# Performance work log

Measured on AMD Instinct MI355X. Metric: run time of the kernel, lower is better.

## Reference

```python
import jax, jax.numpy as jnp
import numpy as np

B, D_IN, H, D_OUT = 2048, 1024, 2048, 1024
MAX_STEPS = 12
EPS = 0.01


def setup_inputs() -> dict:
    key = jax.random.key(0)
    ks = jax.random.split(key, 8)
    s_in = 1.0 / np.sqrt(D_IN + H)
    s_h = 1.0 / np.sqrt(H)
    return {
        "x": jax.random.normal(ks[0], (B, D_IN), jnp.float32),
        "h": jax.random.normal(ks[1], (B, H), jnp.float32),
        "W_hidden": jax.random.normal(ks[2], (H, D_IN + H), jnp.float32) * s_in,
        "b_hidden": jnp.zeros((H,), jnp.float32),
        "w_halt": jax.random.normal(ks[3], (H,), jnp.float32) * s_h,
        "b_halt": jnp.float32(-2.0),  # bias low so several ponder steps are taken
        "W_out": jax.random.normal(ks[4], (D_OUT, H), jnp.float32) * s_h,
        "b_out": jnp.zeros((D_OUT,), jnp.float32),
    }


def reference(x, h, W_hidden, b_hidden, w_halt, b_halt, W_out, b_out):
    # Batched ACT halting loop, unrolled to MAX_STEPS via lax.scan.
    def step(s, t):
        # step 0 of the original uses x+1 as a "first step" flag
        xin = jnp.where(t == 0, x + 1.0, x)          # [B, D_IN]
        z = jnp.concatenate([xin, s], axis=-1)        # [B, D_IN+H]
        s_new = z @ W_hidden.T + b_hidden             # [B, H]
        p = jax.nn.sigmoid(s_new @ w_halt + b_halt)   # [B]
        out = s_new @ W_out.T + b_out                 # [B, D_OUT]
        return s_new, (s_new, p, out)

    _, (states, probs, outs) = jax.lax.scan(step, h, jnp.arange(MAX_STEPS))
    # states: [T,B,H], probs: [T,B], outs: [T,B,D_OUT]

    cum = jnp.cumsum(probs, axis=0)                   # [T,B]
    reached = cum >= (1.0 - EPS)
    # first step where cumulative halt prob crosses the threshold (cap at T-1)
    n = jnp.where(jnp.any(reached, axis=0), jnp.argmax(reached, axis=0), MAX_STEPS - 1)  # [B]

    t_idx = jnp.arange(MAX_STEPS)[:, None]            # [T,1]
    before = t_idx < n[None, :]                       # [T,B]
    R = 1.0 - jnp.sum(jnp.where(before, probs, 0.0), axis=0)  # [B] remainder
    w = jnp.where(before, probs, jnp.where(t_idx == n[None, :], R[None, :], 0.0))  # [T,B]

    output = jnp.einsum("tb,tbd->bd", w, outs)        # [B, D_OUT]
    hidden = jnp.einsum("tb,tbh->bh", w, states)      # [B, H]
    ponder = (n + 1).astype(jnp.float32) + R          # [B]
    return output, hidden, ponder
```

## Files before the change

kernel.cpp:

```cpp
#include <hip/hip_runtime.h>
#include <hip/hip_bf16.h>
#include <cstdint>

#define B_SZ   2048
#define D_INN  1024
#define H_SZ   2048
#define D_OUTN 1024
#define TMAX   12
#define LDW    3072

typedef _Float16 f16;
typedef __attribute__((ext_vector_type(8))) _Float16 f16x8;
typedef __attribute__((ext_vector_type(4))) float    f32x4;

typedef const __attribute__((address_space(1))) uint32_t* gptr_t;
typedef __attribute__((address_space(3))) uint32_t*       lptr_t;
__device__ inline void gld16(const void* g, void* l) {
    __builtin_amdgcn_global_load_lds((gptr_t)g, (lptr_t)l, 16, 0, 0);
}

template<int BN>
__global__ __launch_bounds__(512, 4) void gemm16(
    const f16* __restrict__ A, int lda,
    const f16* __restrict__ Bm, int ldb,
    const float* __restrict__ Cadd,
    const float* __restrict__ radd,
    float* __restrict__ Cf,
    f16* __restrict__ Cs,
    float* __restrict__ hid,
    const float* __restrict__ wvec,
    int hacc,
    f16* __restrict__ hid16,
    int ldc, int K, int nx)
{
    constexpr int WN = BN / 64;
    constexpr int NV = (BN == 128) ? 3 : 2;
    __shared__ __align__(16) f16 As[3][64 * 64];
    __shared__ __align__(16) f16 Bs[3][BN * 64];
    const int tid  = threadIdx.x;
    const int wave = tid >> 6;
    const int lane = tid & 63;

    const int nwg = gridDim.x;
    const int cpx = nwg >> 3;
    const int bid = (blockIdx.x & 7) * cpx + (blockIdx.x >> 3);
    const int m0 = (bid / nx) * 64, n0 = (bid % nx) * BN;

    const int wr = wave >> 2, wc = wave & 3;
    const int fr = lane & 15, fq = lane >> 4;

    const int acs = tid ^ ((tid >> 3) & 7);
    const f16* gA = A + (size_t)(m0 + (acs >> 3)) * lda + (acs & 7) * 8;
    const int adst = wave << 9;
    const int bcs1 = tid ^ ((tid >> 3) & 7);
    const f16* gB1 = Bm + (size_t)(n0 + (bcs1 >> 3)) * ldb + (bcs1 & 7) * 8;
    const int bdst1 = wave << 9;
    const f16* gB2 = nullptr;
    int bdst2 = 0;
    if constexpr (BN == 128) {
        const int bc2 = tid + 512;
        const int bcs2 = bc2 ^ ((bc2 >> 3) & 7);
        gB2 = Bm + (size_t)(n0 + (bcs2 >> 3)) * ldb + (bcs2 & 7) * 8;
        bdst2 = 4096 + (wave << 9);
    }

    int offA[2][2], offB[WN][2];
#pragma unroll
    for (int m = 0; m < 2; ++m)
#pragma unroll
        for (int ks = 0; ks < 2; ++ks) {
            const int row = wr * 32 + m * 16 + fr;
            offA[m][ks] = row * 64 + (((ks * 4 + fq) ^ (row & 7)) << 3);
        }
#pragma unroll
    for (int n = 0; n < WN; ++n)
#pragma unroll
        for (int ks = 0; ks < 2; ++ks) {
            const int row = wc * (WN * 16) + n * 16 + fr;
            offB[n][ks] = row * 64 + (((ks * 4 + fq) ^ (row & 7)) << 3);
        }

    auto STAGE = [&](int buf, int ko) {
        gld16(gA + ko,  &As[buf][0] + adst);
        gld16(gB1 + ko, &Bs[buf][0] + bdst1);
        if constexpr (BN == 128) gld16(gB2 + ko, &Bs[buf][0] + bdst2);
    };

    f32x4 acc[2][WN] = {};

    STAGE(0, 0);
    const int nk = K >> 6;
    int cur = 0;
    for (int ki = 0; ki < nk; ++ki) {
        const int nxt = (cur == 2) ? 0 : cur + 1;
        if (ki + 1 < nk) {
            STAGE(nxt, (ki + 1) << 6);
            asm volatile("s_waitcnt vmcnt(%0)" :: "i"(NV) : "memory");
        } else {
            asm volatile("s_waitcnt vmcnt(0)" ::: "memory");
        }
        __builtin_amdgcn_s_barrier();
        asm volatile("" ::: "memory");

        f16x8 a[2][2], b[WN][2];
#pragma unroll
        for (int m = 0; m < 2; ++m)
#pragma unroll
            for (int ks = 0; ks < 2; ++ks)
                a[m][ks] = *(const f16x8*)(&As[cur][offA[m][ks]]);
#pragma unroll
        for (int n = 0; n < WN; ++n)
#pragma unroll
            for (int ks = 0; ks < 2; ++ks)
                b[n][ks] = *(const f16x8*)(&Bs[cur][offB[n][ks]]);
#pragma unroll
        for (int ks = 0; ks < 2; ++ks)
#pragma unroll
            for (int m = 0; m < 2; ++m)
#pragma unroll
                for (int n = 0; n < WN; ++n)
                    acc[m][n] = __builtin_amdgcn_mfma_f32_16x16x32_f16(
                        a[m][ks], b[n][ks], acc[m][n], 0, 0, 0);
        cur = nxt;
    }

    float wr8[2][4];
    if (hid) {
#pragma unroll
        for (int m = 0; m < 2; ++m)
#pragma unroll
            for (int r = 0; r < 4; ++r)
                wr8[m][r] = wvec[m0 + wr * 32 + m * 16 + fq * 4 + r];
    }
#pragma unroll
    for (int m = 0; m < 2; ++m) {
#pragma unroll
        for (int n = 0; n < WN; ++n) {
#pragma unroll
            for (int r = 0; r < 4; ++r) {
                const int row = m0 + wr * 32 + m * 16 + fq * 4 + r;
                const int col = n0 + wc * (WN * 16) + n * 16 + fr;
                const size_t o = (size_t)row * ldc + col;
                float v = acc[m][n][r];
                if (Cadd) v += Cadd[o];
                if (radd) v += radd[col];
                if (Cf) Cf[o] = v;
                if (Cs) Cs[o] = (f16)v;
                if (hid) {
                    const float hv = hacc ? hid[o] + wr8[m][r] * v
                                          : wr8[m][r] * v;
                    hid[o] = hv;
                    if (hid16) hid16[o] = (f16)hv;
                }
            }
        }
    }
}

__global__ __launch_bounds__(256) void cast16(
    const float* __restrict__ src, int ld, int cols,
    f16* __restrict__ dst, int total8)
{
    const int i = blockIdx.x * 256 + threadIdx.x;
    if (i >= total8) return;
    const int idx = i * 8;
    const int r = idx / cols, c = idx % cols;
    const float4 v0 = *(const float4*)(src + (size_t)r * ld + c);
    const float4 v1 = *(const float4*)(src + (size_t)r * ld + c + 4);
    f16x8 o;
    o[0]=(f16)v0.x; o[1]=(f16)v0.y; o[2]=(f16)v0.z; o[3]=(f16)v0.w;
    o[4]=(f16)v1.x; o[5]=(f16)v1.y; o[6]=(f16)v1.z; o[7]=(f16)v1.w;
    *(f16x8*)(dst + idx) = o;
}

__global__ __launch_bounds__(256) void rowsum_kernel(
    const float* __restrict__ W, int ld, int K, float* __restrict__ out)
{
    const int j = blockIdx.x;
    const int tid = threadIdx.x;
    float s = 0.f;
    for (int k = tid; k < K; k += 256) s += W[(size_t)j * ld + k];
#pragma unroll
    for (int off = 32; off; off >>= 1) s += __shfl_down(s, off);
    __shared__ float red[4];
    if ((tid & 63) == 0) red[tid >> 6] = s;
    __syncthreads();
    if (tid == 0) out[j] = red[0] + red[1] + red[2] + red[3];
}

__global__ __launch_bounds__(256) void transpose_w(
    const float* __restrict__ in, float* __restrict__ out, int R, int C)
{
    __shared__ float t[32][33];
    const int bc = blockIdx.x * 32, br = blockIdx.y * 32;
    const int tx = threadIdx.x & 31, ty = threadIdx.x >> 5;
#pragma unroll
    for (int i = 0; i < 32; i += 8)
        t[ty + i][tx] = in[(size_t)(br + ty + i) * C + bc + tx];
    __syncthreads();
#pragma unroll
    for (int i = 0; i < 32; i += 8)
        out[(size_t)(bc + ty + i) * R + br + tx] = t[tx][ty + i];
}

__global__ __launch_bounds__(256) void init_u0(
    const float* __restrict__ w, double* __restrict__ u)
{
    const int i = blockIdx.x * 256 + threadIdx.x;
    if (i < H_SZ) u[i] = (double)w[i];
}

__global__ __launch_bounds__(256) void gemv_t(
    const float* __restrict__ WT, const double* __restrict__ uin,
    double* __restrict__ uout)
{
    const int i = blockIdx.x;
    const int tid = threadIdx.x;
    const float* row = WT + (size_t)(D_INN + i) * H_SZ;
    double acc = 0.0;
    for (int j = tid; j < H_SZ; j += 256) acc += (double)row[j] * uin[j];
#pragma unroll
    for (int off = 32; off; off >>= 1) acc += __shfl_down(acc, off);
    __shared__ double red[4];
    if ((tid & 63) == 0) red[tid >> 6] = acc;
    __syncthreads();
    if (tid == 0) uout[i] = red[0] + red[1] + red[2] + red[3];
}

__global__ __launch_bounds__(256) void batch_wx(
    const float* __restrict__ WT, const double* __restrict__ U,
    double* __restrict__ XU, double* __restrict__ XS)
{
    const int k = blockIdx.x;
    const int tid = threadIdx.x;
    const float* row = WT + (size_t)k * H_SZ;
    double au[TMAX] = {}, av[TMAX] = {};
    for (int j = tid; j < H_SZ; j += 256) {
        const double w = (double)row[j];
        double pref = 0.0;
#pragma unroll
        for (int t = 0; t < TMAX; ++t) {
            const double u = U[(size_t)t * H_SZ + j];
            pref += u;
            au[t] += w * u;
            av[t] += w * pref;
        }
    }
    __shared__ double red[4][2 * TMAX];
#pragma unroll
    for (int t = 0; t < TMAX; ++t) {
#pragma unroll
        for (int off = 32; off; off >>= 1) {
            au[t] += __shfl_down(au[t], off);
            av[t] += __shfl_down(av[t], off);
        }
    }
    if ((tid & 63) == 0) {
#pragma unroll
        for (int t = 0; t < TMAX; ++t) {
            red[tid >> 6][t] = au[t];
            red[tid >> 6][TMAX + t] = av[t];
        }
    }
    __syncthreads();
    if (tid == 0) {
#pragma unroll
        for (int t = 0; t < TMAX; ++t) {
            XS[(size_t)t * D_INN + k] = red[0][t] + red[1][t] + red[2][t] + red[3][t];
            XU[(size_t)t * D_INN + k] = red[0][TMAX+t] + red[1][TMAX+t]
                                      + red[2][TMAX+t] + red[3][TMAX+t];
        }
    }
}

__global__ __launch_bounds__(256) void e_kernel(
    const double* __restrict__ XS, const double* __restrict__ U,
    const float* __restrict__ bh, double* __restrict__ E)
{
    const int t = blockIdx.x;
    const int tid = threadIdx.x;
    double a = 0.0;
    for (int k = tid; k < D_INN; k += 256) a += XS[(size_t)t * D_INN + k];
    for (int j = tid; j < H_SZ; j += 256) {
        double v = 0.0;
        for (int s = 0; s <= t; ++s) v += U[(size_t)s * H_SZ + j];
        a += v * (double)bh[j];
    }
#pragma unroll
    for (int off = 32; off; off >>= 1) a += __shfl_down(a, off);
    __shared__ double red[4];
    if ((tid & 63) == 0) red[tid >> 6] = a;
    __syncthreads();
    if (tid == 0) E[t] = red[0] + red[1] + red[2] + red[3];
}

__global__ __launch_bounds__(256) void d_kernel(
    const float* __restrict__ h, const float* __restrict__ x,
    const double* __restrict__ U, const double* __restrict__ XU,
    const double* __restrict__ E, double* __restrict__ Dm)
{
    const int b = blockIdx.x;
    const int tid = threadIdx.x;
    double acc[TMAX] = {};
    for (int i = tid; i < H_SZ; i += 256) {
        const double hv = (double)h[(size_t)b * H_SZ + i];
#pragma unroll
        for (int t = 0; t < TMAX; ++t)
            acc[t] += hv * U[(size_t)(t + 1) * H_SZ + i];
    }
    for (int i = tid; i < D_INN; i += 256) {
        const double xv = (double)x[(size_t)b * D_INN + i];
#pragma unroll
        for (int t = 0; t < TMAX; ++t)
            acc[t] += xv * XU[(size_t)t * D_INN + i];
    }
    __shared__ double red[4][TMAX];
#pragma unroll
    for (int t = 0; t < TMAX; ++t)
#pragma unroll
        for (int off = 32; off; off >>= 1) acc[t] += __shfl_down(acc[t], off);
    if ((tid & 63) == 0)
#pragma unroll
        for (int t = 0; t < TMAX; ++t) red[tid >> 6][t] = acc[t];
    __syncthreads();
    if (tid == 0)
#pragma unroll
        for (int t = 0; t < TMAX; ++t)
            Dm[(size_t)b * TMAX + t] =
                red[0][t] + red[1][t] + red[2][t] + red[3][t] + E[t];
}

__global__ __launch_bounds__(256) void sched_kernel(
    const double* __restrict__ Dm, const float* __restrict__ b_halt,
    float* __restrict__ Wmat, float* __restrict__ ponder)
{
    const int b = blockIdx.x * 256 + threadIdx.x;
    if (b >= B_SZ) return;
    const float bh = b_halt[0];
    float cum = 0.f, R = 0.f;
    int n = -1;
    float w[TMAX];
#pragma unroll
    for (int t = 0; t < TMAX; ++t) {
        const float p = 1.f / (1.f + expf(-((float)Dm[(size_t)b * TMAX + t] + bh)));
        if (n < 0) {
            const float c = cum + p;
            if (c >= 0.99f || t == TMAX - 1) { n = t; R = 1.f - cum; w[t] = R; }
            else { w[t] = p; cum = c; }
        } else {
            w[t] = 0.f;
        }
    }
    ponder[b] = (float)(n + 1) + R;
#pragma unroll
    for (int t = 0; t < TMAX; ++t) Wmat[(size_t)t * B_SZ + b] = w[t];
}

extern "C" void kernel_launch(void* const* d_in, const int* in_sizes, int n_in,
                              void* d_out, int out_size, void* d_ws, size_t ws_size,
                              hipStream_t stream)
{
    const float* x        = (const float*)d_in[0];
    const float* h        = (const float*)d_in[1];
    const float* W_hidden = (const float*)d_in[2];
    const float* b_hidden = (const float*)d_in[3];
    const float* w_halt   = (const float*)d_in[4];
    const float* b_halt   = (const float*)d_in[5];
    const float* W_out    = (const float*)d_in[6];
    const float* b_out    = (const float*)d_in[7];

    float* out    = (float*)d_out;
    float* output = out;
    float* hidden = out + (size_t)B_SZ * D_OUTN;
    float* ponder = hidden + (size_t)B_SZ * H_SZ;

    double* U   = (double*)d_ws;
    double* XU  = U  + (size_t)(TMAX + 1) * H_SZ;
    double* XS  = XU + (size_t)TMAX * D_INN;
    double* E   = XS + (size_t)TMAX * D_INN;
    double* Dm  = E + 16;
    float* rsum = (float*)(Dm + (size_t)B_SZ * TMAX);
    float* Wmat = rsum + H_SZ;
    float* WT   = Wmat + (size_t)TMAX * B_SZ;
    float* xc   = WT;
    f16* xh   = (f16*)(WT + (size_t)LDW * H_SZ);
    f16* Wxh  = xh  + (size_t)B_SZ * D_INN;
    f16* sh0  = Wxh + (size_t)H_SZ * D_INN;
    f16* sh1  = sh0 + (size_t)B_SZ * H_SZ;
    f16* Wsh  = sh1 + (size_t)B_SZ * H_SZ;
    f16* Woh  = Wsh + (size_t)H_SZ * H_SZ;
    f16* hid16 = xh;

    const dim3 blk(256);
    const dim3 gblk(512);

    cast16<<<dim3(B_SZ * D_INN / 8 / 256), blk, 0, stream>>>(
        x, D_INN, D_INN, xh, B_SZ * D_INN / 8);
    cast16<<<dim3(B_SZ * H_SZ / 8 / 256), blk, 0, stream>>>(
        h, H_SZ, H_SZ, sh0, B_SZ * H_SZ / 8);
    cast16<<<dim3(H_SZ * D_INN / 8 / 256), blk, 0, stream>>>(
        W_hidden, LDW, D_INN, Wxh, H_SZ * D_INN / 8);
    cast16<<<dim3(H_SZ * H_SZ / 8 / 256), blk, 0, stream>>>(
        W_hidden + D_INN, LDW, H_SZ, Wsh, H_SZ * H_SZ / 8);
    cast16<<<dim3(D_OUTN * H_SZ / 8 / 256), blk, 0, stream>>>(
        W_out, H_SZ, H_SZ, Woh, D_OUTN * H_SZ / 8);

    rowsum_kernel<<<dim3(H_SZ), blk, 0, stream>>>(W_hidden, LDW, D_INN, rsum);

    transpose_w<<<dim3(LDW / 32, H_SZ / 32), blk, 0, stream>>>(
        W_hidden, WT, H_SZ, LDW);
    init_u0<<<dim3(H_SZ / 256), blk, 0, stream>>>(w_halt, U);
    for (int k = 0; k < TMAX; ++k)
        gemv_t<<<dim3(H_SZ), blk, 0, stream>>>(WT, U + (size_t)k * H_SZ,
                                               U + (size_t)(k + 1) * H_SZ);
    batch_wx<<<dim3(D_INN), blk, 0, stream>>>(WT, U, XU, XS);
    e_kernel<<<dim3(TMAX), blk, 0, stream>>>(XS, U, b_hidden, E);
    d_kernel<<<dim3(B_SZ), blk, 0, stream>>>(h, x, U, XU, E, Dm);
    sched_kernel<<<dim3(B_SZ / 256), blk, 0, stream>>>(Dm, b_halt, Wmat, ponder);

    gemm16<128><<<dim3((B_SZ / 64) * (H_SZ / 128)), gblk, 0, stream>>>(
        xh, D_INN, Wxh, D_INN, nullptr, b_hidden, xc, nullptr,
        nullptr, nullptr, 0, nullptr, H_SZ, D_INN, H_SZ / 128);

    for (int t = 0; t < TMAX; ++t) {
        const f16* ph = (t & 1) ? sh1 : sh0;
        f16*       nh = (t & 1) ? sh0 : sh1;
        gemm16<128><<<dim3((B_SZ / 64) * (H_SZ / 128)), gblk, 0, stream>>>(
            ph, H_SZ, Wsh, H_SZ, xc, (t == 0) ? rsum : nullptr,
            nullptr, nh, hidden, Wmat + (size_t)t * B_SZ, (t > 0),
            (t == TMAX - 1) ? hid16 : nullptr, H_SZ, H_SZ, H_SZ / 128);
    }

    gemm16<64><<<dim3((B_SZ / 64) * (D_OUTN / 64)), gblk, 0, stream>>>(
        hid16, H_SZ, Woh, H_SZ, nullptr, b_out, output, nullptr,
        nullptr, nullptr, 0, nullptr, D_OUTN, H_SZ, D_OUTN / 64);
}
```

Before: 604.3 us.

## Store x-projection in fp16, skip zero-weight hidden updates, split halting dot kernel

The precomputed x·Wx^T + b term is now stored as fp16 and read as fp16 in each of the 12 recurrent GEMM epilogues, halving that per-step read traffic. The hidden accumulation skips the read-modify-write when the row's halting weight is zero. The per-row halting-logit kernel is restructured into column slices with the U coefficients staged in LDS, and partial sums are reduced in the scheduling kernel. Storing the x-term in fp16 adds rounding error to every recurrent step.

```diff
diff --git a/kernel.cpp b/kernel.cpp
--- a/kernel.cpp
+++ b/kernel.cpp
@@ -8,6 +8,8 @@
 #define D_OUTN 1024
 #define TMAX   12
 #define LDW    3072
+#define NSL    12
+#define SLC    256
 
 typedef _Float16 f16;
 typedef __attribute__((ext_vector_type(8))) _Float16 f16x8;
@@ -24,6 +26,7 @@
     const f16* __restrict__ A, int lda,
     const f16* __restrict__ Bm, int ldb,
     const float* __restrict__ Cadd,
+    const f16*  __restrict__ Cadd16,
     const float* __restrict__ radd,
     float* __restrict__ Cf,
     f16* __restrict__ Cs,
@@ -142,15 +145,24 @@
                 const int col = n0 + wc * (WN * 16) + n * 16 + fr;
                 const size_t o = (size_t)row * ldc + col;
                 float v = acc[m][n][r];
-                if (Cadd) v += Cadd[o];
-                if (radd) v += radd[col];
+                if (Cadd)   v += Cadd[o];
+                if (Cadd16) v += (float)Cadd16[o];
+                if (radd)   v += radd[col];
                 if (Cf) Cf[o] = v;
                 if (Cs) Cs[o] = (f16)v;
                 if (hid) {
-                    const float hv = hacc ? hid[o] + wr8[m][r] * v
-                                          : wr8[m][r] * v;
-                    hid[o] = hv;
-                    if (hid16) hid16[o] = (f16)hv;
+                    const float w = wr8[m][r];
+                    if (!hacc) {
+                        const float hv = w * v;
+                        hid[o] = hv;
+                        if (hid16) hid16[o] = (f16)hv;
+                    } else if (w != 0.f) {
+                        const float hv = hid[o] + w * v;
+                        hid[o] = hv;
+                        if (hid16) hid16[o] = (f16)hv;
+                    } else if (hid16) {
+                        hid16[o] = (f16)hid[o];
+                    }
                 }
             }
         }
@@ -294,44 +306,50 @@
     if (tid == 0) E[t] = red[0] + red[1] + red[2] + red[3];
 }
 
-__global__ __launch_bounds__(256) void d_kernel(
+__global__ __launch_bounds__(256) void d_part(
     const float* __restrict__ h, const float* __restrict__ x,
     const double* __restrict__ U, const double* __restrict__ XU,
-    const double* __restrict__ E, double* __restrict__ Dm)
-{
-    const int b = blockIdx.x;
+    double* __restrict__ part)
+{
+    __shared__ double Us[TMAX][SLC];
+    const int blk = blockIdx.x;
+    const int sl  = blk % NSL;
+    const int br  = (blk / NSL) * 32;
     const int tid = threadIdx.x;
+    const int col0 = sl * SLC;
+    const bool isH = col0 < H_SZ;
+#pragma unroll
+    for (int t = 0; t < TMAX; ++t)
+        Us[t][tid] = isH ? U[(size_t)(t + 1) * H_SZ + col0 + tid]
+                         : XU[(size_t)t * D_INN + (col0 - H_SZ) + tid];
+    __syncthreads();
+    const int lane8 = tid & 7;
+    const int row   = tid >> 3;
+    const float* src = isH ? (h + (size_t)(br + row) * H_SZ + col0)
+                           : (x + (size_t)(br + row) * D_INN + (col0 - H_SZ));
     double acc[TMAX] = {};
-    for (int i = tid; i < H_SZ; i += 256) {
-        const double hv = (double)h[(size_t)b * H_SZ + i];
+    const int c0 = lane8 * 32;
+    for (int c = c0; c < c0 + 32; ++c) {
+        const double v = (double)src[c];
+#pragma unroll
+        for (int t = 0; t < TMAX; ++t) acc[t] += v * Us[t][c];
+    }
+#pragma unroll
+    for (int t = 0; t < TMAX; ++t) {
+        acc[t] += __shfl_xor(acc[t], 1, 64);
+        acc[t] += __shfl_xor(acc[t], 2, 64);
+        acc[t] += __shfl_xor(acc[t], 4, 64);
+    }
+    if (lane8 == 0) {
 #pragma unroll
         for (int t = 0; t < TMAX; ++t)
-            acc[t] += hv * U[(size_t)(t + 1) * H_SZ + i];
-    }
-    for (int i = tid; i < D_INN; i += 256) {
-        const double xv = (double)x[(size_t)b * D_INN + i];
-#pragma unroll
-        for (int t = 0; t < TMAX; ++t)
-            acc[t] += xv * XU[(size_t)t * D_INN + i];
-    }
-    __shared__ double red[4][TMAX];
-#pragma unroll
-    for (int t = 0; t < TMAX; ++t)
-#pragma unroll
-        for (int off = 32; off; off >>= 1) acc[t] += __shfl_down(acc[t], off);
-    if ((tid & 63) == 0)
-#pragma unroll
-        for (int t = 0; t < TMAX; ++t) red[tid >> 6][t] = acc[t];
-    __syncthreads();
-    if (tid == 0)
-#pragma unroll
-        for (int t = 0; t < TMAX; ++t)
-            Dm[(size_t)b * TMAX + t] =
-                red[0][t] + red[1][t] + red[2][t] + red[3][t] + E[t];
+            part[((size_t)(br + row) * NSL + sl) * TMAX + t] = acc[t];
+    }
 }
 
 __global__ __launch_bounds__(256) void sched_kernel(
-    const double* __restrict__ Dm, const float* __restrict__ b_halt,
+    const double* __restrict__ part, const double* __restrict__ E,
+    const float* __restrict__ b_halt,
     float* __restrict__ Wmat, float* __restrict__ ponder)
 {
     const int b = blockIdx.x * 256 + threadIdx.x;
@@ -342,7 +360,11 @@
     float w[TMAX];
 #pragma unroll
     for (int t = 0; t < TMAX; ++t) {
-        const float p = 1.f / (1.f + expf(-((float)Dm[(size_t)b * TMAX + t] + bh)));
+        double dd = E[t];
+#pragma unroll
+        for (int sl = 0; sl < NSL; ++sl)
+            dd += part[((size_t)b * NSL + sl) * TMAX + t];
+        const float p = 1.f / (1.f + expf(-((float)dd + bh)));
         if (n < 0) {
             const float c = cum + p;
             if (c >= 0.99f || t == TMAX - 1) { n = t; R = 1.f - cum; w[t] = R; }
@@ -374,21 +396,21 @@
     float* hidden = out + (size_t)B_SZ * D_OUTN;
     float* ponder = hidden + (size_t)B_SZ * H_SZ;
 
-    double* U   = (double*)d_ws;
-    double* XU  = U  + (size_t)(TMAX + 1) * H_SZ;
-    double* XS  = XU + (size_t)TMAX * D_INN;
-    double* E   = XS + (size_t)TMAX * D_INN;
-    double* Dm  = E + 16;
-    float* rsum = (float*)(Dm + (size_t)B_SZ * TMAX);
-    float* Wmat = rsum + H_SZ;
-    float* WT   = Wmat + (size_t)TMAX * B_SZ;
-    float* xc   = WT;
+    double* U    = (double*)d_ws;
+    double* XU   = U  + (size_t)(TMAX + 1) * H_SZ;
+    double* XS   = XU + (size_t)TMAX * D_INN;
+    double* E    = XS + (size_t)TMAX * D_INN;
+    double* part = E + 16;
+    float* rsum  = (float*)(part + (size_t)B_SZ * NSL * TMAX);
+    float* Wmat  = rsum + H_SZ;
+    float* WT    = Wmat + (size_t)TMAX * B_SZ;
     f16* xh   = (f16*)(WT + (size_t)LDW * H_SZ);
     f16* Wxh  = xh  + (size_t)B_SZ * D_INN;
     f16* sh0  = Wxh + (size_t)H_SZ * D_INN;
     f16* sh1  = sh0 + (size_t)B_SZ * H_SZ;
     f16* Wsh  = sh1 + (size_t)B_SZ * H_SZ;
     f16* Woh  = Wsh + (size_t)H_SZ * H_SZ;
+    f16* xc16 = Woh + (size_t)D_OUTN * H_SZ;
     f16* hid16 = xh;
 
     const dim3 blk(256);
@@ -415,23 +437,24 @@
                                                U + (size_t)(k + 1) * H_SZ);
     batch_wx<<<dim3(D_INN), blk, 0, stream>>>(WT, U, XU, XS);
     e_kernel<<<dim3(TMAX), blk, 0, stream>>>(XS, U, b_hidden, E);
-    d_kernel<<<dim3(B_SZ), blk, 0, stream>>>(h, x, U, XU, E, Dm);
-    sched_kernel<<<dim3(B_SZ / 256), blk, 0, stream>>>(Dm, b_halt, Wmat, ponder);
+    d_part<<<dim3((B_SZ / 32) * NSL), blk, 0, stream>>>(h, x, U, XU, part);
+    sched_kernel<<<dim3(B_SZ / 256), blk, 0, stream>>>(part, E, b_halt,
+                                                       Wmat, ponder);
 
     gemm16<128><<<dim3((B_SZ / 64) * (H_SZ / 128)), gblk, 0, stream>>>(
-        xh, D_INN, Wxh, D_INN, nullptr, b_hidden, xc, nullptr,
+        xh, D_INN, Wxh, D_INN, nullptr, nullptr, b_hidden, nullptr, xc16,
         nullptr, nullptr, 0, nullptr, H_SZ, D_INN, H_SZ / 128);
 
     for (int t = 0; t < TMAX; ++t) {
         const f16* ph = (t & 1) ? sh1 : sh0;
         f16*       nh = (t & 1) ? sh0 : sh1;
         gemm16<128><<<dim3((B_SZ / 64) * (H_SZ / 128)), gblk, 0, stream>>>(
-            ph, H_SZ, Wsh, H_SZ, xc, (t == 0) ? rsum : nullptr,
+            ph, H_SZ, Wsh, H_SZ, nullptr, xc16, (t == 0) ? rsum : nullptr,
             nullptr, nh, hidden, Wmat + (size_t)t * B_SZ, (t > 0),
             (t == TMAX - 1) ? hid16 : nullptr, H_SZ, H_SZ, H_SZ / 128);
     }
 
     gemm16<64><<<dim3((B_SZ / 64) * (D_OUTN / 64)), gblk, 0, stream>>>(
-        hid16, H_SZ, Woh, H_SZ, nullptr, b_out, output, nullptr,
+        hid16, H_SZ, Woh, H_SZ, nullptr, nullptr, b_out, output, nullptr,
         nullptr, nullptr, 0, nullptr, D_OUTN, H_SZ, D_OUTN / 64);
 }
```

After: 619.2 us. 1.02x slower.
